# Kernel tuning notes

Hardware: AMD Instinct MI355X
Metric: run time of the kernel (lower is better)

## Reference

```python
import jax, jax.numpy as jnp
import numpy as np

NUM_HEADS = 16


def rotate_half(x):
    x1 = x[..., ::2]
    x2 = x[..., 1::2]
    return jnp.concatenate((-x2, x1), axis=-1)


def rope_sin_cos(seq_len, head_dim, dtype):
    inv_freq = 1.0 / (10000.0 ** (jnp.arange(0, head_dim, 2, dtype=jnp.float32) / head_dim))
    t = jnp.arange(seq_len, dtype=jnp.float32)
    freqs = jnp.einsum('i,j->ij', t, inv_freq)          # [S, D/2]
    emb = jnp.concatenate((freqs, freqs), axis=-1)      # [S, D]
    return jnp.sin(emb).astype(dtype), jnp.cos(emb).astype(dtype)


def setup_inputs() -> dict:
    key = jax.random.key(0)
    B, S, E = 2, 2048, 2048
    ks = jax.random.split(key, 5)
    scale = 1.0 / np.sqrt(E)
    return {
        'x': jax.random.normal(ks[0], (B, S, E), dtype=jnp.float32),
        'mask': jnp.ones((B, S), dtype=jnp.int32),
        'Wq': jax.random.normal(ks[1], (E, E), dtype=jnp.float32) * scale,
        'bq': jnp.zeros((E,), dtype=jnp.float32),
        'Wk': jax.random.normal(ks[2], (E, E), dtype=jnp.float32) * scale,
        'bk': jnp.zeros((E,), dtype=jnp.float32),
        'Wv': jax.random.normal(ks[3], (E, E), dtype=jnp.float32) * scale,
        'bv': jnp.zeros((E,), dtype=jnp.float32),
        'Wo': jax.random.normal(ks[4], (E, E), dtype=jnp.float32) * scale,
        'bo': jnp.zeros((E,), dtype=jnp.float32),
    }


def reference(x, mask, Wq, bq, Wk, bk, Wv, bv, Wo, bo):
    B, S, E = x.shape
    H = NUM_HEADS
    D = E // H
    q = (x @ Wq + bq).reshape(B, S, H, D).transpose(0, 2, 1, 3)  # [B,H,S,D]
    k = (x @ Wk + bk).reshape(B, S, H, D).transpose(0, 2, 1, 3)
    v = (x @ Wv + bv).reshape(B, S, H, D).transpose(0, 2, 1, 3)

    sin, cos = rope_sin_cos(S, D, q.dtype)  # [S,D]
    sin = sin[None, None]                    # [1,1,S,D]
    cos = cos[None, None]
    q = q * cos + rotate_half(q) * sin
    k = k * cos + rotate_half(k) * sin

    scores = jnp.einsum('bhqd,bhkd->bhqk', q, k) / jnp.sqrt(jnp.asarray(D, q.dtype))
    scores = jnp.where(mask[:, None, None, :] == 0, -jnp.inf, scores)
    probs = jax.nn.softmax(scores, axis=-1)
    attn = jnp.einsum('bhqk,bhkd->bhqd', probs, v)       # [B,H,S,D]
    attn = attn.transpose(0, 2, 1, 3).reshape(B, S, E)
    return attn @ Wo + bo
```

## Files before the change

### kernel.cpp

```cpp
#include <hip/hip_runtime.h>
#include <hip/hip_bf16.h>
#include <cmath>

typedef unsigned short u16;
typedef unsigned int   u32;

using v4f    = __attribute__((ext_vector_type(4)))  float;
using f32x16 = __attribute__((ext_vector_type(16))) float;
using s8v    = __attribute__((ext_vector_type(8)))  short;
using u32x2  = __attribute__((ext_vector_type(2)))  unsigned int;

union Frag { uint4 u; s8v s; };

__device__ __forceinline__ u16 f2bf(float f){
  u32 u = __float_as_uint(f);
  u32 r = u + 0x7fffu + ((u >> 16) & 1u);
  return (u16)(r >> 16);
}
__device__ __forceinline__ float bf2f(u16 h){ return __uint_as_float(((u32)h) << 16); }

__device__ __forceinline__ u32 cvtpk(float a, float b){
  u32 r;
  asm("v_cvt_pk_bf16_f32 %0, %1, %2" : "=v"(r) : "v"(a), "v"(b));
  return r;
}

__device__ __forceinline__ void async16(const void* g, void* l){
  __builtin_amdgcn_global_load_lds((__attribute__((address_space(1))) void*)g,
                                   (__attribute__((address_space(3))) void*)l, 16, 0, 0);
}

__global__ __launch_bounds__(256) void prep_kernel(
    const float* __restrict__ x, u16* __restrict__ xb,
    const float* __restrict__ W0, const float* __restrict__ W1,
    const float* __restrict__ W2, const float* __restrict__ W3,
    u16* __restrict__ T0, u16* __restrict__ T1, u16* __restrict__ T2, u16* __restrict__ T3){
  __shared__ float tile[64][65];
  const int bid = blockIdx.x;
  if (bid < 8192){
    size_t i = ((size_t)bid * 256 + threadIdx.x) * 4;
    float4 v = *(const float4*)(x + i);
    uint2 o;
    o.x = (u32)f2bf(v.x) | ((u32)f2bf(v.y) << 16);
    o.y = (u32)f2bf(v.z) | ((u32)f2bf(v.w) << 16);
    *(uint2*)(xb + i) = o;
    return;
  }
  const int t4 = bid - 8192;
  const int z  = t4 >> 10;
  const float* W = (z==0)?W0:(z==1)?W1:(z==2)?W2:W3;
  u16*         T = (z==0)?T0:(z==1)?T1:(z==2)?T2:T3;
  const int k0 = ((t4 & 1023) >> 5)*64, n0 = (t4 & 31)*64;
  const int t  = threadIdx.x;
  const int rr = t >> 4, c4 = (t & 15) * 4;
  #pragma unroll
  for (int i=0;i<4;i++){
    int k = rr + i*16;
    float4 v = *(const float4*)(W + (size_t)(k0+k)*2048 + n0 + c4);
    tile[k][c4+0]=v.x; tile[k][c4+1]=v.y; tile[k][c4+2]=v.z; tile[k][c4+3]=v.w;
  }
  __syncthreads();
  #pragma unroll
  for (int i=0;i<4;i++){
    int n = rr + i*16;
    uint2 o;
    o.x = (u32)f2bf(tile[c4+0][n]) | ((u32)f2bf(tile[c4+1][n])<<16);
    o.y = (u32)f2bf(tile[c4+2][n]) | ((u32)f2bf(tile[c4+3][n])<<16);
    *(uint2*)(T + (size_t)(n0+n)*2048 + k0 + c4) = o;
  }
}

template<int MODE>
__device__ __forceinline__ void gemm_tile(const u16* __restrict__ A, const u16* __restrict__ BT,
                                          const float* __restrict__ bias, void* __restrict__ Cout,
                                          int m0, int n0, u16* Asl, u16* Bsl){
  constexpr int K = 2048;
  const int tid  = threadIdx.x;
  const int w    = tid >> 6;
  const int lane = tid & 63;
  const int r    = lane & 15, q = lane >> 4;
  const int wm   = (w >> 1) * 64, wn = (w & 1) * 64;

  v4f acc[4][4];
  #pragma unroll
  for (int i=0;i<4;i++)
    #pragma unroll
    for (int j=0;j<4;j++) acc[i][j] = (v4f)0.f;

  const int srow = w*32 + (lane>>3);
  const int sblk = (lane&7) ^ ((lane>>3)&7);
  const u16* Ag = A  + (size_t)(m0+srow)*K + sblk*8;
  const u16* Bg = BT + (size_t)(n0+srow)*K + sblk*8;
  u16* Als = Asl + (w*32)*64;
  u16* Bls = Bsl + (w*32)*64;

  for (int kk = 0; kk < K; kk += 64) {
    #pragma unroll
    for (int i=0;i<4;i++){
      async16(Ag + (size_t)i*8*K + kk, Als + i*512);
      async16(Bg + (size_t)i*8*K + kk, Bls + i*512);
    }
    __syncthreads();
    #pragma unroll
    for (int ks=0; ks<2; ++ks) {
      s8v af[4], bfr[4];
      #pragma unroll
      for (int i=0;i<4;i++){
        int rho = wm + i*16 + r;
        int p = (ks*4 + q) ^ (r&7);
        Frag t; t.u = *(const uint4*)(Asl + rho*64 + p*8); af[i] = t.s;
      }
      #pragma unroll
      for (int j=0;j<4;j++){
        int rho = wn + j*16 + r;
        int p = (ks*4 + q) ^ (r&7);
        Frag t; t.u = *(const uint4*)(Bsl + rho*64 + p*8); bfr[j] = t.s;
      }
      #pragma unroll
      for (int i=0;i<4;i++)
        #pragma unroll
        for (int j=0;j<4;j++)
          acc[i][j] = __builtin_amdgcn_mfma_f32_16x16x32_bf16(af[i], bfr[j], acc[i][j], 0, 0, 0);
    }
    __syncthreads();
  }

  float bv[4];
  #pragma unroll
  for (int j=0;j<4;j++) bv[j] = bias[n0 + wn + j*16 + r];

  #pragma unroll
  for (int i=0;i<4;i++){
    #pragma unroll
    for (int j=0;j<4;j++){
      const int gn = n0 + wn + j*16 + r;
      #pragma unroll
      for (int rr2=0; rr2<4; ++rr2){
        const int gm = m0 + wm + i*16 + q*4 + rr2;
        float val = acc[i][j][rr2] + bv[j];
        if (MODE == 0) ((u16*)Cout)[(size_t)gm*2048 + gn] = f2bf(val);
        else           ((float*)Cout)[(size_t)gm*2048 + gn] = val;
      }
    }
  }
}

__global__ __launch_bounds__(256) void gemm_qkv_kernel(
    const u16* __restrict__ A,
    const u16* __restrict__ WqT, const u16* __restrict__ WkT, const u16* __restrict__ WvT,
    const float* __restrict__ bq, const float* __restrict__ bk, const float* __restrict__ bv,
    u16* __restrict__ Qb, u16* __restrict__ Kb, u16* __restrict__ Vb){
  __shared__ u16 Asl[128*64];
  __shared__ u16 Bsl[128*64];
  const int L   = blockIdx.x + 48*blockIdx.y;
  const int wid = (L & 7)*192 + (L >> 3);
  const int bx  = wid % 48, by = wid / 48;
  const int mat = bx >> 4;
  const u16*   BT   = (mat==0)?WqT:(mat==1)?WkT:WvT;
  const float* bias = (mat==0)?bq :(mat==1)?bk :bv;
  u16*         Cout = (mat==0)?Qb :(mat==1)?Kb :Vb;
  gemm_tile<0>(A, BT, bias, Cout, by*128, (bx & 15)*128, Asl, Bsl);
}

__global__ __launch_bounds__(256) void gemm_wo_kernel(const u16* __restrict__ A,
                                                      const u16* __restrict__ WoT,
                                                      const float* __restrict__ bias,
                                                      float* __restrict__ out){
  __shared__ u16 Asl[128*64];
  __shared__ u16 Bsl[128*64];
  const int L   = blockIdx.x + 16*blockIdx.y;
  const int wid = (L & 7)*64 + (L >> 3);
  const int bx  = wid % 16, by = wid / 16;
  gemm_tile<1>(A, WoT, bias, out, by*128, bx*128, Asl, Bsl);
}

__global__ __launch_bounds__(256) void rope_tv_kernel(u16* __restrict__ Q, u16* __restrict__ Kb,
                                                      const u16* __restrict__ V, u16* __restrict__ VT){
  __shared__ u16 t[64*72];
  const int bid = blockIdx.x;
  if (bid < 32768){
    const int ry = bid >> 14;
    const int rx = bid & 16383;
    const int wrow = rx*4 + (threadIdx.x >> 6);
    const int lane = threadIdx.x & 63;
    u16* P = (ry == 0) ? Q : Kb;
    const int s = (wrow >> 4) & 2047;
    const size_t base = (size_t)wrow * 128;
    float invf = exp2f(-(float)lane * 0.20762050593045952f);
    float angle = (float)s * invf;
    float sn, cs;
    sincosf(angle, &sn, &cs);
    float x_j   = bf2f(P[base + lane]);
    float x_j64 = bf2f(P[base + 64 + lane]);
    float x_2j  = bf2f(P[base + 2*lane]);
    float x_2j1 = bf2f(P[base + 2*lane + 1]);
    float o0 = x_j  * cs - x_2j1 * sn;
    float o1 = x_j64 * cs + x_2j  * sn;
    P[base + lane]      = f2bf(o0);
    P[base + 64 + lane] = f2bf(o1);
    return;
  }
  const int tb = bid - 32768;
  const int s0 = (tb & 31)*64;
  const int d0 = ((tb >> 5) & 1)*64;
  const int bh = tb >> 6;
  const int b = bh >> 4, h = bh & 15;
  const size_t obase = ((size_t)bh*128 + d0)*2048 + s0;
  const int tid = threadIdx.x;
  #pragma unroll
  for (int i=0;i<2;i++){
    int c = tid + i*256;
    int sl = c >> 3, dc = (c & 7) * 8;
    *(uint4*)(t + sl*72 + dc) =
      *(const uint4*)(V + ((size_t)(b*2048 + s0 + sl))*2048 + h*128 + d0 + dc);
  }
  __syncthreads();
  #pragma unroll
  for (int i=0;i<2;i++){
    int c = tid + i*256;
    int dl = c >> 3, sc4 = (c & 7) * 8;
    u16 tmp[8];
    #pragma unroll
    for (int j=0;j<8;j++) tmp[j] = t[(sc4+j)*72 + dl];
    *(uint4*)(VT + obase + (size_t)dl*2048 + sc4) = *(const uint4*)tmp;
  }
}

__global__ __launch_bounds__(256,2) void attn_kernel(const u16* __restrict__ Q,
                                                     const u16* __restrict__ K,
                                                     const u16* __restrict__ VT,
                                                     const int* __restrict__ mask,
                                                     u16* __restrict__ Out){
  constexpr int S = 2048;
  constexpr float SL2 = 0.08838834764831845f * 1.4426950408889634f;
  __shared__ u16 smem[32768];

  const int tid = threadIdx.x, w = tid >> 6, lane = tid & 63;
  const int qc = lane & 31;
  const int h  = lane >> 5;
  const int l7 = lane & 7;
  const int hh = blockIdx.y, b = blockIdx.z;
  const int q0 = blockIdx.x * 128;
  const size_t rowb = (size_t)b * 2048;
  const size_t bhD  = ((size_t)(b*16 + hh)) * 128;

  s8v qf[8];
  {
    const u16* qp = Q + (rowb + q0 + w*32 + qc)*2048 + hh*128 + h*8;
    #pragma unroll
    for (int t=0;t<8;t++){ Frag f; f.u = *(const uint4*)(qp + t*16); qf[t] = f.s; }
  }

  f32x16 accO[4];
  #pragma unroll
  for (int d=0; d<4; d++) accO[d] = (f32x16)0.f;
  float lsum = 0.f;

  const int sr4 = lane >> 4, sp16 = lane & 15;
  const int vr8 = lane >> 3, vp8 = lane & 7;

  auto stage = [&](u16* base, int key0){
    u16* Kd = base;
    u16* Vd = base + 8192;
    #pragma unroll
    for (int i=0;i<4;i++){
      int R = w*16 + i*4;
      int ob = sp16 ^ ((R&7) + sr4);
      async16(K + (rowb + key0 + R + sr4)*2048 + hh*128 + ob*8, Kd + R*128);
    }
    #pragma unroll
    for (int i=0;i<4;i++){
      int R = w*32 + i*8;
      int ob = vp8 ^ vr8;
      async16(VT + (bhD + R + vr8)*2048 + key0 + ob*8, Vd + R*64);
    }
  };

  stage(smem, 0);
  int mv = mask[b*S + lane];
  __syncthreads();
  unsigned long long bm = __ballot(mv != 0);
  int cur = 0;

  for (int it=0; it<32; ++it){
    if (it < 31){
      stage(smem + (cur^1)*16384, (it+1)*64);
      mv = mask[b*S + (it+1)*64 + lane];
    }
    const u16* Ks = smem + cur*16384;
    const u16* Vs = Ks + 8192;

    #pragma unroll
    for (int nb=0; nb<2; ++nb){
      f32x16 sc = (f32x16)0.f;
      __builtin_amdgcn_s_setprio(1);
      #pragma unroll
      for (int t=0;t<8;t++){
        Frag kf; kf.u = *(const uint4*)(Ks + (nb*32 + qc)*128 + (((2*t + h) ^ l7)*8));
        sc = __builtin_amdgcn_mfma_f32_32x32x16_bf16(kf.s, qf[t], sc, 0, 0, 0);
      }
      __builtin_amdgcn_s_setprio(0);
      float p[16];
      #pragma unroll
      for (int m=0; m<16; ++m) p[m] = exp2f(sc[m] * SL2);
      if (bm != ~0ull){
        #pragma unroll
        for (int m=0; m<16; ++m){
          int bit = nb*32 + (m&3) + 8*(m>>2) + 4*h;
          if (!((bm >> bit) & 1ull)) p[m] = 0.f;
        }
      }
      #pragma unroll
      for (int m=0; m<16; ++m) lsum += p[m];

      #pragma unroll
      for (int g=0; g<2; ++g){
        u32 a0 = cvtpk(p[8*g+0], p[8*g+1]);
        u32 a1 = cvtpk(p[8*g+2], p[8*g+3]);
        u32 a2 = cvtpk(p[8*g+4], p[8*g+5]);
        u32 a3 = cvtpk(p[8*g+6], p[8*g+7]);
        u32x2 r0 = __builtin_amdgcn_permlane32_swap(a0, a2, false, false);
        u32x2 r1 = __builtin_amdgcn_permlane32_swap(a1, a3, false, false);
        Frag pf; pf.u = make_uint4(r0[0], r1[0], r0[1], r1[1]);
        const int T = nb*2 + g;
        __builtin_amdgcn_s_setprio(1);
        #pragma unroll
        for (int d=0; d<4; ++d){
          Frag vf; vf.u = *(const uint4*)(Vs + (d*32 + qc)*64 + (((2*T + h) ^ l7)*8));
          accO[d] = __builtin_amdgcn_mfma_f32_32x32x16_bf16(vf.s, pf.s, accO[d], 0, 0, 0);
        }
        __builtin_amdgcn_s_setprio(0);
      }
    }
    __syncthreads();
    bm = __ballot(mv != 0);
    cur ^= 1;
  }

  float sall = lsum + __shfl_xor(lsum, 32, 64);
  float invv = (sall > 0.f) ? 1.f/sall : 0.f;
  u16* orow = Out + (rowb + q0 + w*32 + qc)*2048 + hh*128;
  #pragma unroll
  for (int d=0; d<4; ++d){
    #pragma unroll
    for (int g2=0; g2<4; ++g2){
      uint2 o;
      o.x = cvtpk(accO[d][g2*4+0] * invv, accO[d][g2*4+1] * invv);
      o.y = cvtpk(accO[d][g2*4+2] * invv, accO[d][g2*4+3] * invv);
      *(uint2*)(orow + d*32 + g2*8 + 4*h) = o;
    }
  }
}

extern "C" void kernel_launch(void* const* d_in, const int* in_sizes, int n_in,
                              void* d_out, int out_size, void* d_ws, size_t ws_size,
                              hipStream_t stream) {
  (void)in_sizes; (void)n_in; (void)out_size; (void)ws_size;
  const float* x    = (const float*)d_in[0];
  const int*   mask = (const int*)d_in[1];
  const float* Wq   = (const float*)d_in[2];
  const float* bq   = (const float*)d_in[3];
  const float* Wk   = (const float*)d_in[4];
  const float* bk   = (const float*)d_in[5];
  const float* Wv   = (const float*)d_in[6];
  const float* bv   = (const float*)d_in[7];
  const float* Wo   = (const float*)d_in[8];
  const float* bo   = (const float*)d_in[9];

  u16* xbf = (u16*)d_ws;
  u16* WqT = xbf + 8388608;
  u16* WkT = WqT + 4194304;
  u16* WvT = WkT + 4194304;
  u16* WoT = WvT + 4194304;
  u16* Qb  = WoT + 4194304;
  u16* Kb  = Qb + 8388608;
  u16* Vb  = Kb + 8388608;
  u16* VTb = Vb + 8388608;
  u16* Ab  = VTb + 8388608;

  prep_kernel<<<12288, 256, 0, stream>>>(x, xbf, Wq, Wk, Wv, Wo, WqT, WkT, WvT, WoT);
  gemm_qkv_kernel<<<dim3(48,32), 256, 0, stream>>>(xbf, WqT, WkT, WvT, bq, bk, bv, Qb, Kb, Vb);
  rope_tv_kernel<<<34816, 256, 0, stream>>>(Qb, Kb, Vb, VTb);
  attn_kernel<<<dim3(16,16,2), 256, 0, stream>>>(Qb, Kb, VTb, mask, Ab);
  gemm_wo_kernel<<<dim3(16,32), 256, 0, stream>>>(Ab, WoT, bo, (float*)d_out);
}
```

Measured before the change: 419.6 us.

## Fuse RoPE into QKV GEMM epilogue and drop tile swizzle

Applies the rotary embedding to Q and K inside the QKV GEMM epilogue: the output tile is staged in shared memory and rotated before being written to global memory. The RoPE pass over Q/K is removed from the separate kernel, which now only transposes V. This avoids a full read-modify-write of Q and K. The grouped block-index remapping in both GEMM kernels is also removed, which can reduce L2 reuse of the A and B tiles.

```diff
diff --git a/kernel.cpp b/kernel.cpp
--- a/kernel.cpp
+++ b/kernel.cpp
@@ -73,8 +73,10 @@
 template<int MODE>
 __device__ __forceinline__ void gemm_tile(const u16* __restrict__ A, const u16* __restrict__ BT,
                                           const float* __restrict__ bias, void* __restrict__ Cout,
-                                          int m0, int n0, u16* Asl, u16* Bsl){
+                                          int m0, int n0, u16* sm){
   constexpr int K = 2048;
+  u16* Asl = sm;
+  u16* Bsl = sm + 8192;
   const int tid  = threadIdx.x;
   const int w    = tid >> 6;
   const int lane = tid & 63;
@@ -129,18 +131,46 @@
   #pragma unroll
   for (int j=0;j<4;j++) bv[j] = bias[n0 + wn + j*16 + r];
 
-  #pragma unroll
-  for (int i=0;i<4;i++){
-    #pragma unroll
-    for (int j=0;j<4;j++){
-      const int gn = n0 + wn + j*16 + r;
-      #pragma unroll
-      for (int rr2=0; rr2<4; ++rr2){
-        const int gm = m0 + wm + i*16 + q*4 + rr2;
-        float val = acc[i][j][rr2] + bv[j];
-        if (MODE == 0) ((u16*)Cout)[(size_t)gm*2048 + gn] = f2bf(val);
-        else           ((float*)Cout)[(size_t)gm*2048 + gn] = val;
-      }
+  if constexpr (MODE != 3){
+    #pragma unroll
+    for (int i=0;i<4;i++){
+      #pragma unroll
+      for (int j=0;j<4;j++){
+        const int gn = n0 + wn + j*16 + r;
+        #pragma unroll
+        for (int rr2=0; rr2<4; ++rr2){
+          const int gm = m0 + wm + i*16 + q*4 + rr2;
+          float val = acc[i][j][rr2] + bv[j];
+          if (MODE == 0) ((u16*)Cout)[(size_t)gm*2048 + gn] = f2bf(val);
+          else           ((float*)Cout)[(size_t)gm*2048 + gn] = val;
+        }
+      }
+    }
+  } else {
+    #pragma unroll
+    for (int i=0;i<4;i++)
+      #pragma unroll
+      for (int j=0;j<4;j++){
+        const int col = wn + j*16 + r;
+        #pragma unroll
+        for (int rr2=0; rr2<4; ++rr2)
+          sm[(wm + i*16 + q*4 + rr2)*128 + col] = f2bf(acc[i][j][rr2] + bv[j]);
+      }
+    __syncthreads();
+    const float invf = exp2f(-(float)lane * 0.20762050593045952f);
+    for (int rr=0; rr<32; ++rr){
+      const int row = w*32 + rr;
+      const int s = (m0 + row) & 2047;
+      float sn, cs;
+      sincosf((float)s * invf, &sn, &cs);
+      const u16* tr = sm + row*128;
+      float x_j   = bf2f(tr[lane]);
+      float x_j64 = bf2f(tr[64 + lane]);
+      float x_2j  = bf2f(tr[2*lane]);
+      float x_2j1 = bf2f(tr[2*lane + 1]);
+      u16* gp = (u16*)Cout + (size_t)(m0 + row)*2048 + n0;
+      gp[lane]      = f2bf(x_j  * cs - x_2j1 * sn);
+      gp[64 + lane] = f2bf(x_j64 * cs + x_2j  * sn);
     }
   }
 }
@@ -150,57 +180,27 @@
     const u16* __restrict__ WqT, const u16* __restrict__ WkT, const u16* __restrict__ WvT,
     const float* __restrict__ bq, const float* __restrict__ bk, const float* __restrict__ bv,
     u16* __restrict__ Qb, u16* __restrict__ Kb, u16* __restrict__ Vb){
-  __shared__ u16 Asl[128*64];
-  __shared__ u16 Bsl[128*64];
-  const int L   = blockIdx.x + 48*blockIdx.y;
-  const int wid = (L & 7)*192 + (L >> 3);
-  const int bx  = wid % 48, by = wid / 48;
+  __shared__ u16 sm[16384];
+  const int bx = blockIdx.x, by = blockIdx.y;
   const int mat = bx >> 4;
   const u16*   BT   = (mat==0)?WqT:(mat==1)?WkT:WvT;
   const float* bias = (mat==0)?bq :(mat==1)?bk :bv;
   u16*         Cout = (mat==0)?Qb :(mat==1)?Kb :Vb;
-  gemm_tile<0>(A, BT, bias, Cout, by*128, (bx & 15)*128, Asl, Bsl);
+  if (mat < 2) gemm_tile<3>(A, BT, bias, Cout, by*128, (bx & 15)*128, sm);
+  else         gemm_tile<0>(A, BT, bias, Cout, by*128, (bx & 15)*128, sm);
 }
 
 __global__ __launch_bounds__(256) void gemm_wo_kernel(const u16* __restrict__ A,
                                                       const u16* __restrict__ WoT,
                                                       const float* __restrict__ bias,
                                                       float* __restrict__ out){
-  __shared__ u16 Asl[128*64];
-  __shared__ u16 Bsl[128*64];
-  const int L   = blockIdx.x + 16*blockIdx.y;
-  const int wid = (L & 7)*64 + (L >> 3);
-  const int bx  = wid % 16, by = wid / 16;
-  gemm_tile<1>(A, WoT, bias, out, by*128, bx*128, Asl, Bsl);
-}
-
-__global__ __launch_bounds__(256) void rope_tv_kernel(u16* __restrict__ Q, u16* __restrict__ Kb,
-                                                      const u16* __restrict__ V, u16* __restrict__ VT){
+  __shared__ u16 sm[16384];
+  gemm_tile<1>(A, WoT, bias, out, blockIdx.y*128, blockIdx.x*128, sm);
+}
+
+__global__ __launch_bounds__(256) void tv_kernel(const u16* __restrict__ V, u16* __restrict__ VT){
   __shared__ u16 t[64*72];
-  const int bid = blockIdx.x;
-  if (bid < 32768){
-    const int ry = bid >> 14;
-    const int rx = bid & 16383;
-    const int wrow = rx*4 + (threadIdx.x >> 6);
-    const int lane = threadIdx.x & 63;
-    u16* P = (ry == 0) ? Q : Kb;
-    const int s = (wrow >> 4) & 2047;
-    const size_t base = (size_t)wrow * 128;
-    float invf = exp2f(-(float)lane * 0.20762050593045952f);
-    float angle = (float)s * invf;
-    float sn, cs;
-    sincosf(angle, &sn, &cs);
-    float x_j   = bf2f(P[base + lane]);
-    float x_j64 = bf2f(P[base + 64 + lane]);
-    float x_2j  = bf2f(P[base + 2*lane]);
-    float x_2j1 = bf2f(P[base + 2*lane + 1]);
-    float o0 = x_j  * cs - x_2j1 * sn;
-    float o1 = x_j64 * cs + x_2j  * sn;
-    P[base + lane]      = f2bf(o0);
-    P[base + 64 + lane] = f2bf(o1);
-    return;
-  }
-  const int tb = bid - 32768;
+  const int tb = blockIdx.x;
   const int s0 = (tb & 31)*64;
   const int d0 = ((tb >> 5) & 1)*64;
   const int bh = tb >> 6;
@@ -380,7 +380,7 @@
 
   prep_kernel<<<12288, 256, 0, stream>>>(x, xbf, Wq, Wk, Wv, Wo, WqT, WkT, WvT, WoT);
   gemm_qkv_kernel<<<dim3(48,32), 256, 0, stream>>>(xbf, WqT, WkT, WvT, bq, bk, bv, Qb, Kb, Vb);
-  rope_tv_kernel<<<34816, 256, 0, stream>>>(Qb, Kb, Vb, VTb);
+  tv_kernel<<<2048, 256, 0, stream>>>(Vb, VTb);
   attn_kernel<<<dim3(16,16,2), 256, 0, stream>>>(Qb, Kb, VTb, mask, Ab);
   gemm_wo_kernel<<<dim3(16,32), 256, 0, stream>>>(Ab, WoT, bo, (float*)d_out);
 }
```

After: 404.3 us. 3.6% less time.
